# Optimization experiments

Measured on AMD Instinct MI355X. Metric: run time of the kernel, lower is better.

The kernel has to match this reference:

```python
import jax, jax.numpy as jnp
import numpy as np

NUM_PARTITIONS = 128
C = 32
D = 128
B, S, K = 4, 2048, 2


def setup_inputs() -> dict:
    key = jax.random.key(0)
    k1, k2, k3, k4 = jax.random.split(key, 4)
    partition_indices = jax.random.randint(k1, (B, S, K), 0, NUM_PARTITIONS)
    keys = jax.random.normal(k2, (B, S, K, C), dtype=jnp.float32)
    values = jax.random.normal(k3, (B, S, D), dtype=jnp.float32)
    queries = jax.random.normal(k4, (B, S, D), dtype=jnp.float32)
    return {
        "partition_indices": partition_indices,
        "keys": keys,
        "values": values,
        "queries": queries,
    }


def reference(partition_indices, keys, values, queries):
    # States start at zero; update() scatter-adds outer(k_bti, v_bt) into
    # states[p_bti]. read() then computes sum_i states[p_bti].mean(axis=0) * q_bt.
    b, s, k, c = keys.shape
    d = values.shape[-1]
    # outer products: [B,S,K,c,d]
    outer = keys[..., :, None] * values[:, :, None, None, :]
    flat_outer = outer.reshape(b * s * k, c, d)
    seg = partition_indices.reshape(-1)
    # scatter-add into partitioned states [P, c, d]
    states = jax.ops.segment_sum(flat_outer, seg, num_segments=NUM_PARTITIONS)
    means = states.mean(axis=1)  # [P, d]
    gathered = means[partition_indices]  # [B, S, K, d]
    out = gathered.sum(axis=2) * queries  # [B, S, d]
    return out
```

## Files before the change

### kernel.cpp

```cpp
#include <hip/hip_runtime.h>
#include <hip/hip_bf16.h>

#define P_  128
#define C_  32
#define D_  128
#define BS_ 8192
#define PD_ (P_*D_)
#define NB_ 256

__global__ __launch_bounds__(512) void scatter_partials(
    const int* __restrict__ idx, const float* __restrict__ keys,
    const float* __restrict__ values, float* __restrict__ partials)
{
    __shared__ float lmeans[PD_];
    float4* lm4 = (float4*)lmeans;
    const int tid = threadIdx.x;
    for (int i = tid; i < PD_ / 4; i += 512) lm4[i] = float4{0.f, 0.f, 0.f, 0.f};
    __syncthreads();

    const int lane = tid & 63;
    const int wave = tid >> 6;
    const int rbase = blockIdx.x * 32 + wave;

    float kv[4], va[4], vb[4];
    int2  ii[4];
    #pragma unroll
    for (int j = 0; j < 4; ++j) {
        const int r = rbase + 8 * j;
        kv[j] = keys[(size_t)r * 64 + lane];
        ii[j] = ((const int2*)idx)[r];
        va[j] = values[(size_t)r * D_ + lane];
        vb[j] = values[(size_t)r * D_ + 64 + lane];
    }

    #pragma unroll
    for (int j = 0; j < 4; ++j) {
        float s = kv[j];
        s += __shfl_xor(s, 16);
        s += __shfl_xor(s, 8);
        s += __shfl_xor(s, 4);
        s += __shfl_xor(s, 2);
        s += __shfl_xor(s, 1);
        const float ks0 = __shfl(s, 0)  * (1.f / 32.f);
        const float ks1 = __shfl(s, 32) * (1.f / 32.f);
        atomicAdd(&lmeans[ii[j].x * D_ + lane],      ks0 * va[j]);
        atomicAdd(&lmeans[ii[j].x * D_ + 64 + lane], ks0 * vb[j]);
        atomicAdd(&lmeans[ii[j].y * D_ + lane],      ks1 * va[j]);
        atomicAdd(&lmeans[ii[j].y * D_ + 64 + lane], ks1 * vb[j]);
    }
    __syncthreads();

    float4* dst = (float4*)(partials + (size_t)blockIdx.x * PD_);
    for (int i = tid; i < PD_ / 4; i += 512) dst[i] = lm4[i];
}

__global__ __launch_bounds__(256) void reduce_partials(
    const float* __restrict__ partials, float* __restrict__ means)
{
    __shared__ float red[4][64];
    const int t  = threadIdx.x;
    const int el = t & 63;
    const int g  = t >> 6;
    const int e  = blockIdx.x * 64 + el;
    float s = 0.f;
    #pragma unroll 8
    for (int j = 0; j < 64; ++j)
        s += partials[(size_t)(g * 64 + j) * PD_ + e];
    red[g][el] = s;
    __syncthreads();
    if (t < 64)
        means[blockIdx.x * 64 + t] = red[0][t] + red[1][t] + red[2][t] + red[3][t];
}

__global__ __launch_bounds__(256) void emit_out(
    const int* __restrict__ idx, const float* __restrict__ means,
    const float* __restrict__ queries, float* __restrict__ out)
{
    const int gid = blockIdx.x * 256 + threadIdx.x;
    const int row = gid >> 5;
    const int d4  = gid & 31;
    const int2 ii = ((const int2*)idx)[row];
    const float4 q = ((const float4*)queries)[gid];
    const float4* m4 = (const float4*)means;
    const float4 a = m4[ii.x * 32 + d4];
    const float4 b = m4[ii.y * 32 + d4];
    float4 o;
    o.x = (a.x + b.x) * q.x;
    o.y = (a.y + b.y) * q.y;
    o.z = (a.z + b.z) * q.z;
    o.w = (a.w + b.w) * q.w;
    ((float4*)out)[gid] = o;
}

extern "C" void kernel_launch(void* const* d_in, const int* in_sizes, int n_in,
                              void* d_out, int out_size, void* d_ws, size_t ws_size,
                              hipStream_t stream) {
    const int*   idx     = (const int*)d_in[0];
    const float* keys    = (const float*)d_in[1];
    const float* values  = (const float*)d_in[2];
    const float* queries = (const float*)d_in[3];
    float* out = (float*)d_out;
    float* ws  = (float*)d_ws;

    float* partials = ws;
    float* means    = ws + (size_t)NB_ * PD_;

    scatter_partials<<<NB_, 512, 0, stream>>>(idx, keys, values, partials);
    reduce_partials<<<PD_ / 64, 256, 0, stream>>>(partials, means);
    emit_out<<<(BS_ * D_ / 4) / 256, 256, 0, stream>>>(idx, means, queries, out);
}
```

Measured before the change: 88.12 us.

## Replace per-block partial buffers and reduction kernel with global atomic accumulation

Each block now adds its shared-memory partial means directly into a global means buffer with float atomics, after a small zeroing kernel. This drops the 256 x 64KB partials write and the separate reduce kernel that re-read all of it. The cost is 256-way contention on every one of the 16K global addresses, which must be resolved in L2, and the float summation order becomes nondeterministic.

```diff
diff --git a/kernel.cpp b/kernel.cpp
--- a/kernel.cpp
+++ b/kernel.cpp
@@ -8,9 +8,14 @@
 #define PD_ (P_*D_)
 #define NB_ 256
 
-__global__ __launch_bounds__(512) void scatter_partials(
+__global__ __launch_bounds__(256) void zero_means(float* __restrict__ means)
+{
+    ((float4*)means)[blockIdx.x * 256 + threadIdx.x] = float4{0.f, 0.f, 0.f, 0.f};
+}
+
+__global__ __launch_bounds__(512) void scatter_means(
     const int* __restrict__ idx, const float* __restrict__ keys,
-    const float* __restrict__ values, float* __restrict__ partials)
+    const float* __restrict__ values, float* __restrict__ means)
 {
     __shared__ float lmeans[PD_];
     float4* lm4 = (float4*)lmeans;
@@ -50,26 +55,8 @@
     }
     __syncthreads();
 
-    float4* dst = (float4*)(partials + (size_t)blockIdx.x * PD_);
-    for (int i = tid; i < PD_ / 4; i += 512) dst[i] = lm4[i];
-}
-
-__global__ __launch_bounds__(256) void reduce_partials(
-    const float* __restrict__ partials, float* __restrict__ means)
-{
-    __shared__ float red[4][64];
-    const int t  = threadIdx.x;
-    const int el = t & 63;
-    const int g  = t >> 6;
-    const int e  = blockIdx.x * 64 + el;
-    float s = 0.f;
-    #pragma unroll 8
-    for (int j = 0; j < 64; ++j)
-        s += partials[(size_t)(g * 64 + j) * PD_ + e];
-    red[g][el] = s;
-    __syncthreads();
-    if (t < 64)
-        means[blockIdx.x * 64 + t] = red[0][t] + red[1][t] + red[2][t] + red[3][t];
+    for (int i = tid; i < PD_; i += 512)
+        atomicAdd(&means[i], lmeans[i]);
 }
 
 __global__ __launch_bounds__(256) void emit_out(
@@ -99,13 +86,10 @@
     const float* keys    = (const float*)d_in[1];
     const float* values  = (const float*)d_in[2];
     const float* queries = (const float*)d_in[3];
-    float* out = (float*)d_out;
-    float* ws  = (float*)d_ws;
+    float* out   = (float*)d_out;
+    float* means = (float*)d_ws;
 
-    float* partials = ws;
-    float* means    = ws + (size_t)NB_ * PD_;
-
-    scatter_partials<<<NB_, 512, 0, stream>>>(idx, keys, values, partials);
-    reduce_partials<<<PD_ / 64, 256, 0, stream>>>(partials, means);
+    zero_means<<<PD_ / 4 / 256, 256, 0, stream>>>(means);
+    scatter_means<<<NB_, 512, 0, stream>>>(idx, keys, values, means);
     emit_out<<<(BS_ * D_ / 4) / 256, 256, 0, stream>>>(idx, means, queries, out);
 }
```

After: 98.61 us. 11.9% more time.
